# Performance work log

Measured on AMD Instinct MI355X. Metric: run time of the kernel, lower is better.

## Reference

```python
import jax, jax.numpy as jnp
import numpy as np

N, CIN, T, V = 16, 16, 512, 200
K, COUT, H = 3, 64, 64


def setup_inputs() -> dict:
    key = jax.random.key(0)
    ks = jax.random.split(key, 9)
    s = 0.05
    return {
        "x": jax.random.normal(ks[0], (N, CIN, T, V), jnp.float32),
        "A": jax.random.uniform(ks[1], (K, V, V), jnp.float32) / V,
        "W_gcn": jax.random.normal(ks[2], (K * COUT, CIN), jnp.float32) * s,
        "b_gcn": jnp.zeros((K * COUT,), jnp.float32),
        "W_ih": jax.random.normal(ks[3], (4 * H, COUT), jnp.float32) * s,
        "W_hh": jax.random.normal(ks[4], (4 * H, H), jnp.float32) * s,
        "b_ih": jnp.zeros((4 * H,), jnp.float32),
        "b_hh": jnp.zeros((4 * H,), jnp.float32),
        "W_fc": jax.random.normal(ks[5], (1, H), jnp.float32) * s,
        "b_fc": jnp.zeros((1,), jnp.float32),
    }


def reference(x, A, W_gcn, b_gcn, W_ih, W_hh, b_ih, b_hh, W_fc, b_fc):
    n, c, t, v = x.shape
    k = A.shape[0]
    cout = W_gcn.shape[0] // k
    # ConvTemporalGraphical: 1x1 conv -> (n, k*cout, t, v), reshape, adjacency einsum
    y = jnp.einsum('nctv,oc->notv', x, W_gcn) + b_gcn[None, :, None, None]
    y = y.reshape(n, k, cout, t, v)
    y = jnp.einsum('nkctv,kvw->nctw', y, A)  # (n, cout, t, v)
    # mean over node dim, residual=False -> res=0
    y = jnp.mean(y, axis=3)  # (n, cout, t)
    seq = jnp.transpose(y, (2, 0, 1))  # (t, n, cout) time-major for scan

    def step(carry, xt):
        h, ccell = carry
        gates = xt @ W_ih.T + b_ih + h @ W_hh.T + b_hh  # (n, 4H)
        i, f, g, o = jnp.split(gates, 4, axis=-1)  # torch LSTM gate order
        i = jax.nn.sigmoid(i)
        f = jax.nn.sigmoid(f)
        g = jnp.tanh(g)
        o = jax.nn.sigmoid(o)
        ccell = f * ccell + i * g
        h = o * jnp.tanh(ccell)
        return (h, ccell), None

    h0 = jnp.zeros((n, W_hh.shape[1]), x.dtype)
    (h_last, _), _ = jax.lax.scan(step, (h0, h0), seq)
    out = h_last @ W_fc.T + b_fc  # (n, 1)
    return (out, A)
```

## Files before the change

### kernel.cpp

```cpp
#include <hip/hip_runtime.h>
#include <math.h>

#define N_    16
#define CIN_  16
#define T_    512
#define V_    200
#define K_    3
#define COUT_ 64
#define H_    64
#define G_    256

#define WS_A  0
#define WS_SA 640
#define WS_XA 1024
#define WS_XW (WS_XA + N_ * T_ * K_ * CIN_)

typedef __attribute__((ext_vector_type(4))) float f32x4;

__device__ __forceinline__ float fast_sig(float x) {
    return __builtin_amdgcn_rcpf(1.f + __expf(-x));
}
__device__ __forceinline__ float fast_tanh(float x) {
    return fmaf(-2.f, __builtin_amdgcn_rcpf(1.f + __expf(2.f * x)), 1.f);
}

#define NCOPY ((K_ * V_ * V_ + 255) / 256)
__global__ __launch_bounds__(256) void prep_kernel(const float* __restrict__ A,
                                                   float* __restrict__ out,
                                                   float* __restrict__ ws) {
    int b = blockIdx.x;
    if (b < NCOPY) {
        int tid = b * 256 + threadIdx.x;
        if (tid < K_ * V_ * V_) out[16 + tid] = A[tid];
        if (tid < K_ * V_) {
            const float* row = A + (long)tid * V_;
            float s = 0.f;
            for (int w = 0; w < V_; ++w) s += row[w];
            ws[WS_A + tid] = s * (1.0f / V_);
        }
    } else {
        int k = b - NCOPY;
        const float* Ak = A + (long)k * V_ * V_;
        float s = 0.f;
        for (int i = threadIdx.x; i < V_ * V_; i += 256) s += Ak[i];
        #pragma unroll
        for (int m = 1; m < 64; m <<= 1) s += __shfl_xor(s, m);
        __shared__ float red[4];
        if ((threadIdx.x & 63) == 0) red[threadIdx.x >> 6] = s;
        __syncthreads();
        if (threadIdx.x == 0)
            ws[WS_SA + k] = (red[0] + red[1] + red[2] + red[3]) * (1.0f / V_);
    }
}

#define TT 64
#define PADV 204
__global__ __launch_bounds__(256) void xa_kernel(const float* __restrict__ x,
                                                 float* __restrict__ ws) {
    __shared__ __align__(16) float xt[TT * PADV];
    __shared__ __align__(16) float aS[K_ * V_];
    int tid = threadIdx.x;
    int b = blockIdx.x;
    int tchunk = b & 7;
    int ci = (b >> 3) & 15;
    int n = b >> 7;
    int t0 = tchunk * TT;

    for (int i = tid; i < K_ * V_; i += 256) aS[i] = ws[WS_A + i];

    const float4* xg4 =
        (const float4*)(x + ((long)(n * CIN_ + ci) * T_ + t0) * V_);
    for (int j = tid; j < TT * (V_ / 4); j += 256) {
        float4 v = xg4[j];
        int t = j / (V_ / 4), v4 = (j % (V_ / 4)) * 4;
        *(float4*)(xt + t * PADV + v4) = v;
    }
    __syncthreads();

    int t_local = tid & 63;
    int k = tid >> 6;
    if (k < K_) {
        const float* xr = xt + t_local * PADV;
        const float* ar = aS + k * V_;
        float a0 = 0.f, a1 = 0.f, a2 = 0.f, a3 = 0.f;
        #pragma unroll 5
        for (int v4 = 0; v4 < V_; v4 += 4) {
            float4 xv = *(const float4*)(xr + v4);
            float4 av = *(const float4*)(ar + v4);
            a0 = fmaf(xv.x, av.x, a0);
            a1 = fmaf(xv.y, av.y, a1);
            a2 = fmaf(xv.z, av.z, a2);
            a3 = fmaf(xv.w, av.w, a3);
        }
        float s = (a0 + a1) + (a2 + a3);
        ws[WS_XA + ((long)n * T_ + (t0 + t_local)) * (K_ * CIN_) + k * CIN_ + ci] = s;
    }
}

__global__ __launch_bounds__(256) void seqgates_kernel(
    const float* __restrict__ W_gcn, const float* __restrict__ b_gcn,
    const float* __restrict__ W_ih, const float* __restrict__ b_ih,
    const float* __restrict__ b_hh, float* __restrict__ ws) {
    int t = blockIdx.x;
    int tid = threadIdx.x;
    __shared__ float xaS[N_][K_ * CIN_];
    __shared__ __align__(16) float seqS[N_][COUT_];
    __shared__ float saS[K_];

    if (tid < K_) saS[tid] = ws[WS_SA + tid];
    #pragma unroll
    for (int r = 0; r < 3; ++r) {
        int i = tid + r * 256;
        if (i < N_ * K_ * CIN_) {
            int n = i / (K_ * CIN_), kc = i % (K_ * CIN_);
            xaS[n][kc] = ws[WS_XA + (long)(n * T_ + t) * (K_ * CIN_) + kc];
        }
    }
    __syncthreads();

    {
        int n = tid >> 4, c0 = (tid & 15) * 4;
        #pragma unroll
        for (int cc = 0; cc < 4; ++cc) {
            int c = c0 + cc;
            float s = 0.f;
            #pragma unroll
            for (int k = 0; k < K_; ++k) {
                s = fmaf(b_gcn[k * COUT_ + c], saS[k], s);
                const float* wrow = W_gcn + (long)(k * COUT_ + c) * CIN_;
                #pragma unroll
                for (int ci = 0; ci < CIN_; ++ci)
                    s = fmaf(wrow[ci], xaS[n][k * CIN_ + ci], s);
            }
            seqS[n][c] = s;
        }
    }
    __syncthreads();

    {
        int g = tid;
        float acc[N_];
        #pragma unroll
        for (int n = 0; n < N_; ++n) acc[n] = 0.f;
        const float4* wrow4 = (const float4*)(W_ih + (long)g * H_);
        #pragma unroll
        for (int c4 = 0; c4 < H_ / 4; ++c4) {
            float4 w4 = wrow4[c4];
            #pragma unroll
            for (int n = 0; n < N_; ++n) {
                float4 s4 = ((const float4*)seqS[n])[c4];
                acc[n] = fmaf(w4.x, s4.x, acc[n]);
                acc[n] = fmaf(w4.y, s4.y, acc[n]);
                acc[n] = fmaf(w4.z, s4.z, acc[n]);
                acc[n] = fmaf(w4.w, s4.w, acc[n]);
            }
        }
        float bias = b_ih[g] + b_hh[g];
        #pragma unroll
        for (int n = 0; n < N_; ++n)
            ws[WS_XW + (long)(t * N_ + n) * G_ + g] = acc[n] + bias;
    }
}

__global__ __attribute__((amdgpu_waves_per_eu(1, 1)))
__launch_bounds__(256) void lstm_kernel(
    const float* __restrict__ W_hh, const float* __restrict__ W_fc,
    const float* __restrict__ b_fc, const float* __restrict__ ws,
    float* __restrict__ out) {
    int n = blockIdx.x;
    int tid = threadIdx.x;
    int w = tid >> 6;
    int lane = tid & 63;
    int ty = lane >> 4;
    int jj = lane & 15;

    const f32x4* wr = (const f32x4*)(W_hh + (long)(ty * 64 + 16 * w + jj) * H_);
    f32x4 w0, w1, w2, w3, w4, w5, w6, w7, w8, w9, w10, w11, w12, w13, w14, w15;
    #define WLOAD(i) \
        asm volatile("global_load_dwordx4 %0, %1, off" : "=v"(w##i) : "v"(wr + i));
    WLOAD(0)  WLOAD(1)  WLOAD(2)  WLOAD(3)
    WLOAD(4)  WLOAD(5)  WLOAD(6)  WLOAD(7)
    WLOAD(8)  WLOAD(9)  WLOAD(10) WLOAD(11)
    WLOAD(12) WLOAD(13) WLOAD(14) WLOAD(15)
    #undef WLOAD
    asm volatile("s_waitcnt vmcnt(0)" ::: "memory");

    float s_act = (ty == 2) ? 2.f : 1.f;
    float m_act = (ty == 2) ? 2.f : 1.f;
    float b_act = (ty == 2) ? -1.f : 0.f;

    __shared__ __align__(16) float hS[2][H_];
    if (tid < H_) hS[0][tid] = 0.f;
    float ccell = 0.f;
    __syncthreads();

    const float* xw = ws + WS_XW + (long)n * G_ + (ty * 64 + 16 * w + jj);
    float x0 = xw[0];
    float x1 = xw[(long)N_ * G_];

    for (int t = 0; t < T_; ++t) {
        int p = t & 1;
        float gate = x0;
        x0 = x1;
        if (t + 2 < T_) x1 = xw[(long)(t + 2) * N_ * G_];

        float a0 = 0.f, a1 = 0.f, a2 = 0.f, a3 = 0.f;
        const float4* h4 = (const float4*)hS[p];
        #define DOT4(i)                            \
            {                                      \
                float4 hv = h4[i];                 \
                a0 = fmaf(w##i[0], hv.x, a0);      \
                a1 = fmaf(w##i[1], hv.y, a1);      \
                a2 = fmaf(w##i[2], hv.z, a2);      \
                a3 = fmaf(w##i[3], hv.w, a3);      \
            }
        DOT4(0)  DOT4(1)  DOT4(2)  DOT4(3)
        DOT4(4)  DOT4(5)  DOT4(6)  DOT4(7)
        DOT4(8)  DOT4(9)  DOT4(10) DOT4(11)
        DOT4(12) DOT4(13) DOT4(14) DOT4(15)
        #undef DOT4
        gate += (a0 + a1) + (a2 + a3);

        float act = fmaf(m_act, fast_sig(s_act * gate), b_act);
        float fv = __shfl(act, 16 + jj);
        float gv = __shfl(act, 32 + jj);
        float ov = __shfl(act, 48 + jj);
        if (ty == 0) {
            ccell = fmaf(fv, ccell, act * gv);
            float h = ov * fast_tanh(ccell);
            hS[p ^ 1][16 * w + jj] = h;
        }
        __syncthreads();
    }

    if (tid < H_) {
        float pv = hS[0][tid] * W_fc[tid];
        #pragma unroll
        for (int m = 1; m < 64; m <<= 1) pv += __shfl_xor(pv, m);
        if (tid == 0) out[n] = pv + b_fc[0];
    }
}

extern "C" void kernel_launch(void* const* d_in, const int* in_sizes, int n_in,
                              void* d_out, int out_size, void* d_ws, size_t ws_size,
                              hipStream_t stream) {
    const float* x     = (const float*)d_in[0];
    const float* A     = (const float*)d_in[1];
    const float* W_gcn = (const float*)d_in[2];
    const float* b_gcn = (const float*)d_in[3];
    const float* W_ih  = (const float*)d_in[4];
    const float* W_hh  = (const float*)d_in[5];
    const float* b_ih  = (const float*)d_in[6];
    const float* b_hh  = (const float*)d_in[7];
    const float* W_fc  = (const float*)d_in[8];
    const float* b_fc  = (const float*)d_in[9];
    float* out = (float*)d_out;
    float* ws  = (float*)d_ws;

    prep_kernel<<<NCOPY + K_, 256, 0, stream>>>(A, out, ws);
    xa_kernel<<<N_ * CIN_ * (T_ / TT), 256, 0, stream>>>(x, ws);
    seqgates_kernel<<<T_, 256, 0, stream>>>(W_gcn, b_gcn, W_ih, b_ih, b_hh, ws);
    lstm_kernel<<<N_, 256, 0, stream>>>(W_hh, W_fc, b_fc, ws, out);
}
```

Baseline: 351.8 us.

## Collapse LSTM recurrence to one wave per sequence, each lane computing all four gates

Result: slower. 510.7 us (+45.2%).

```diff
diff --git a/kernel.cpp b/kernel.cpp
--- a/kernel.cpp
+++ b/kernel.cpp
@@ -163,81 +163,104 @@
 }
 
 __global__ __attribute__((amdgpu_waves_per_eu(1, 1)))
-__launch_bounds__(256) void lstm_kernel(
+__launch_bounds__(64) void lstm_kernel(
     const float* __restrict__ W_hh, const float* __restrict__ W_fc,
     const float* __restrict__ b_fc, const float* __restrict__ ws,
     float* __restrict__ out) {
     int n = blockIdx.x;
-    int tid = threadIdx.x;
-    int w = tid >> 6;
-    int lane = tid & 63;
-    int ty = lane >> 4;
-    int jj = lane & 15;
-
-    const f32x4* wr = (const f32x4*)(W_hh + (long)(ty * 64 + 16 * w + jj) * H_);
-    f32x4 w0, w1, w2, w3, w4, w5, w6, w7, w8, w9, w10, w11, w12, w13, w14, w15;
-    #define WLOAD(i) \
-        asm volatile("global_load_dwordx4 %0, %1, off" : "=v"(w##i) : "v"(wr + i));
-    WLOAD(0)  WLOAD(1)  WLOAD(2)  WLOAD(3)
-    WLOAD(4)  WLOAD(5)  WLOAD(6)  WLOAD(7)
-    WLOAD(8)  WLOAD(9)  WLOAD(10) WLOAD(11)
-    WLOAD(12) WLOAD(13) WLOAD(14) WLOAD(15)
+    int j = threadIdx.x;
+
+    const f32x4* ra = (const f32x4*)(W_hh + (long)(0 * H_ + j) * H_);
+    const f32x4* rb = (const f32x4*)(W_hh + (long)(1 * H_ + j) * H_);
+    const f32x4* rc = (const f32x4*)(W_hh + (long)(2 * H_ + j) * H_);
+    const f32x4* rd = (const f32x4*)(W_hh + (long)(3 * H_ + j) * H_);
+    f32x4 wa0, wa1, wa2, wa3, wa4, wa5, wa6, wa7, wa8, wa9, wa10, wa11, wa12, wa13, wa14, wa15;
+    f32x4 wb0, wb1, wb2, wb3, wb4, wb5, wb6, wb7, wb8, wb9, wb10, wb11, wb12, wb13, wb14, wb15;
+    f32x4 wc0, wc1, wc2, wc3, wc4, wc5, wc6, wc7, wc8, wc9, wc10, wc11, wc12, wc13, wc14, wc15;
+    f32x4 wd0, wd1, wd2, wd3, wd4, wd5, wd6, wd7, wd8, wd9, wd10, wd11, wd12, wd13, wd14, wd15;
+    #define WLOAD(dst, src, i) \
+        asm volatile("global_load_dwordx4 %0, %1, off" : "=v"(dst##i) : "v"(src + i));
+    #define WLOAD16(dst, src) \
+        WLOAD(dst, src, 0)  WLOAD(dst, src, 1)  WLOAD(dst, src, 2)  WLOAD(dst, src, 3)  \
+        WLOAD(dst, src, 4)  WLOAD(dst, src, 5)  WLOAD(dst, src, 6)  WLOAD(dst, src, 7)  \
+        WLOAD(dst, src, 8)  WLOAD(dst, src, 9)  WLOAD(dst, src, 10) WLOAD(dst, src, 11) \
+        WLOAD(dst, src, 12) WLOAD(dst, src, 13) WLOAD(dst, src, 14) WLOAD(dst, src, 15)
+    WLOAD16(wa, ra)
+    WLOAD16(wb, rb)
+    WLOAD16(wc, rc)
+    WLOAD16(wd, rd)
+    #undef WLOAD16
     #undef WLOAD
     asm volatile("s_waitcnt vmcnt(0)" ::: "memory");
 
-    float s_act = (ty == 2) ? 2.f : 1.f;
-    float m_act = (ty == 2) ? 2.f : 1.f;
-    float b_act = (ty == 2) ? -1.f : 0.f;
-
     __shared__ __align__(16) float hS[2][H_];
-    if (tid < H_) hS[0][tid] = 0.f;
+    hS[0][j] = 0.f;
     float ccell = 0.f;
-    __syncthreads();
-
-    const float* xw = ws + WS_XW + (long)n * G_ + (ty * 64 + 16 * w + jj);
-    float x0 = xw[0];
-    float x1 = xw[(long)N_ * G_];
+
+    const float* xw = ws + WS_XW + (long)n * G_ + j;
+    float xc0 = xw[0],   xc1 = xw[64],  xc2 = xw[128], xc3 = xw[192];
+    const float* xw1 = xw + (long)N_ * G_;
+    float xn0 = xw1[0],  xn1 = xw1[64], xn2 = xw1[128], xn3 = xw1[192];
 
     for (int t = 0; t < T_; ++t) {
         int p = t & 1;
-        float gate = x0;
-        x0 = x1;
-        if (t + 2 < T_) x1 = xw[(long)(t + 2) * N_ * G_];
-
         float a0 = 0.f, a1 = 0.f, a2 = 0.f, a3 = 0.f;
+        float b0 = 0.f, b1 = 0.f, b2 = 0.f, b3 = 0.f;
+        float c0 = 0.f, c1 = 0.f, c2 = 0.f, c3 = 0.f;
+        float d0 = 0.f, d1 = 0.f, d2 = 0.f, d3 = 0.f;
         const float4* h4 = (const float4*)hS[p];
-        #define DOT4(i)                            \
+        #define DOT16(i)                           \
             {                                      \
                 float4 hv = h4[i];                 \
-                a0 = fmaf(w##i[0], hv.x, a0);      \
-                a1 = fmaf(w##i[1], hv.y, a1);      \
-                a2 = fmaf(w##i[2], hv.z, a2);      \
-                a3 = fmaf(w##i[3], hv.w, a3);      \
+                a0 = fmaf(wa##i[0], hv.x, a0);     \
+                a1 = fmaf(wa##i[1], hv.y, a1);     \
+                a2 = fmaf(wa##i[2], hv.z, a2);     \
+                a3 = fmaf(wa##i[3], hv.w, a3);     \
+                b0 = fmaf(wb##i[0], hv.x, b0);     \
+                b1 = fmaf(wb##i[1], hv.y, b1);     \
+                b2 = fmaf(wb##i[2], hv.z, b2);     \
+                b3 = fmaf(wb##i[3], hv.w, b3);     \
+                c0 = fmaf(wc##i[0], hv.x, c0);     \
+                c1 = fmaf(wc##i[1], hv.y, c1);     \
+                c2 = fmaf(wc##i[2], hv.z, c2);     \
+                c3 = fmaf(wc##i[3], hv.w, c3);     \
+                d0 = fmaf(wd##i[0], hv.x, d0);     \
+                d1 = fmaf(wd##i[1], hv.y, d1);     \
+                d2 = fmaf(wd##i[2], hv.z, d2);     \
+                d3 = fmaf(wd##i[3], hv.w, d3);     \
             }
-        DOT4(0)  DOT4(1)  DOT4(2)  DOT4(3)
-        DOT4(4)  DOT4(5)  DOT4(6)  DOT4(7)
-        DOT4(8)  DOT4(9)  DOT4(10) DOT4(11)
-        DOT4(12) DOT4(13) DOT4(14) DOT4(15)
-        #undef DOT4
-        gate += (a0 + a1) + (a2 + a3);
-
-        float act = fmaf(m_act, fast_sig(s_act * gate), b_act);
-        float fv = __shfl(act, 16 + jj);
-        float gv = __shfl(act, 32 + jj);
-        float ov = __shfl(act, 48 + jj);
-        if (ty == 0) {
-            ccell = fmaf(fv, ccell, act * gv);
-            float h = ov * fast_tanh(ccell);
-            hS[p ^ 1][16 * w + jj] = h;
-        }
-        __syncthreads();
-    }
-
-    if (tid < H_) {
-        float pv = hS[0][tid] * W_fc[tid];
+        DOT16(0)  DOT16(1)  DOT16(2)  DOT16(3)
+        DOT16(4)  DOT16(5)  DOT16(6)  DOT16(7)
+        DOT16(8)  DOT16(9)  DOT16(10) DOT16(11)
+        DOT16(12) DOT16(13) DOT16(14) DOT16(15)
+        #undef DOT16
+
+        float gi = xc0 + (a0 + a1) + (a2 + a3);
+        float gf = xc1 + (b0 + b1) + (b2 + b3);
+        float gg = xc2 + (c0 + c1) + (c2 + c3);
+        float go = xc3 + (d0 + d1) + (d2 + d3);
+
+        xc0 = xn0; xc1 = xn1; xc2 = xn2; xc3 = xn3;
+        if (t + 2 < T_) {
+            const float* xw2 = xw + (long)(t + 2) * N_ * G_;
+            xn0 = xw2[0]; xn1 = xw2[64]; xn2 = xw2[128]; xn3 = xw2[192];
+        }
+
+        float iv = fast_sig(gi);
+        float fv = fast_sig(gf);
+        float gv = fast_tanh(gg);
+        float ov = fast_sig(go);
+        ccell = fmaf(fv, ccell, iv * gv);
+        float h = ov * fast_tanh(ccell);
+        hS[p ^ 1][j] = h;
+    }
+
+    {
+        float h = hS[0][j];
+        float pv = h * W_fc[j];
         #pragma unroll
         for (int m = 1; m < 64; m <<= 1) pv += __shfl_xor(pv, m);
-        if (tid == 0) out[n] = pv + b_fc[0];
+        if (j == 0) out[n] = pv + b_fc[0];
     }
 }
 
@@ -260,5 +283,5 @@
     prep_kernel<<<NCOPY + K_, 256, 0, stream>>>(A, out, ws);
     xa_kernel<<<N_ * CIN_ * (T_ / TT), 256, 0, stream>>>(x, ws);
     seqgates_kernel<<<T_, 256, 0, stream>>>(W_gcn, b_gcn, W_ih, b_ih, b_hh, ws);
-    lstm_kernel<<<N_, 256, 0, stream>>>(W_hh, W_fc, b_fc, ws, out);
-}
+    lstm_kernel<<<N_, 64, 0, stream>>>(W_hh, W_fc, b_fc, ws, out);
+}
```
